# Kernel tuning notes

Measured on AMD Instinct MI355X. Metric: run time of the kernel, lower is better.

The kernel has to match this reference:

```python
import jax, jax.numpy as jnp
import numpy as np

IMG = 8       # image_size
LH = 150      # l_h
LQ = 10       # l_q
K = 10        # value-iteration steps
B = 16384     # batch
N_STATES = 2 + IMG * IMG


def _conv(x, w, pad):
    # NCHW conv, stride 1
    return jax.lax.conv_general_dilated(
        x, w, window_strides=(1, 1), padding=[(pad, pad), (pad, pad)],
        dimension_numbers=('NCHW', 'OIHW', 'NCHW'))


def setup_inputs() -> dict:
    key = jax.random.key(0)
    ks = jax.random.split(key, 8)
    grid = jax.random.normal(ks[0], (B, IMG * IMG), dtype=jnp.float32)
    pos = jax.random.randint(ks[1], (B, 2), 0, IMG).astype(jnp.float32)
    S = jnp.concatenate([grid, pos], axis=1)                      # [B, 66]
    Wh = jax.random.normal(ks[2], (LH, 1, 3, 3), jnp.float32) * 0.1
    bh = jnp.zeros((LH,), jnp.float32)
    Wr = jax.random.normal(ks[3], (1, LH, 1, 1), jnp.float32) * 0.1
    Wq = jax.random.normal(ks[4], (LQ, 1, 3, 3), jnp.float32) * 0.1
    w = jax.random.normal(ks[5], (LQ, 1, 3, 3), jnp.float32) * 0.1
    Wfc = jax.random.normal(ks[6], (8, LQ), jnp.float32) * 0.1
    return {'S': S, 'Wh': Wh, 'bh': bh, 'Wr': Wr, 'Wq': Wq, 'w': w, 'Wfc': Wfc}


def reference(S, Wh, bh, Wr, Wq, w, Wfc):
    X = S[:, :IMG * IMG].reshape(-1, 1, IMG, IMG)                 # [B,1,8,8]
    s1 = S[:, IMG * IMG].astype(jnp.int32)                        # row index
    s2 = S[:, IMG * IMG + 1].astype(jnp.int32)                    # col index

    h = _conv(X, Wh, 1) + bh[None, :, None, None]                 # [B,150,8,8]
    r = _conv(h, Wr, 0)                                           # [B,1,8,8]
    q = _conv(r, Wq, 1)                                           # [B,10,8,8]
    v = jnp.max(q, axis=1, keepdims=True)                         # [B,1,8,8]

    Wcat = jnp.concatenate([Wq, w], axis=1)                       # [10,2,3,3]

    def step(v, _):
        qq = _conv(jnp.concatenate([r, v], axis=1), Wcat, 1)
        return jnp.max(qq, axis=1, keepdims=True), None

    v, _ = jax.lax.scan(step, v, None, length=K - 1)
    q = _conv(jnp.concatenate([r, v], axis=1), Wcat, 1)           # [B,10,8,8]

    bidx = jnp.arange(q.shape[0])
    q_sel = q[bidx, :, s1, s2]                                    # [B,10]
    logits = q_sel @ Wfc.T                                        # [B,8]
    return logits
```

## Files before the change

kernel.cpp:

```cpp
#include <hip/hip_runtime.h>

#define IMG 8
#define LH 150
#define LQ 10
#define KITER 10
#define ROW (IMG * IMG + 2)

#define DPP_SHR1 0x111
#define DPP_SHL1 0x101
#define DPP_SHR8 0x118
#define DPP_SHL8 0x108
template <int CTRL>
__device__ __forceinline__ float dppf(float v) {
    return __builtin_bit_cast(float,
        __builtin_amdgcn_update_dpp(0, __builtin_bit_cast(int, v),
                                    CTRL, 0xF, 0xF, true));
}

__device__ __forceinline__ float bperm(int byte_addr, float v) {
    return __builtin_bit_cast(float,
        __builtin_amdgcn_ds_bpermute(byte_addr, __builtin_bit_cast(int, v)));
}

__global__ void weff_kernel(const float* __restrict__ Wh,
                            const float* __restrict__ bh,
                            const float* __restrict__ Wr,
                            float* __restrict__ ws) {
    const int wv = threadIdx.x >> 6;
    const int lane = threadIdx.x & 63;
    float partial = 0.f;
    for (int c = lane; c < LH; c += 64) {
        const float wr = Wr[c];
        partial += wr * ((wv < 9) ? Wh[c * 9 + wv] : bh[c]);
    }
    #pragma unroll
    for (int off = 32; off > 0; off >>= 1)
        partial += __shfl_xor(partial, off);
    if (lane == 0) ws[wv] = partial;
}

__global__ __launch_bounds__(256, 4) void vin_kernel(
    const float* __restrict__ S,
    const float* __restrict__ Wq,
    const float* __restrict__ w,
    const float* __restrict__ Wfc,
    const float* __restrict__ ws,
    float* __restrict__ out,
    int B) {
    const int wave = threadIdx.x >> 6;
    const int lane = threadIdx.x & 63;
    const long wid = (long)blockIdx.x * 4 + wave;
    if (wid * 4 >= B) return;

    const int x = lane & 7;
    const int ioff = (lane >> 4) * ROW;
    const float mskL = (x == 0) ? 0.f : 1.f;
    const float mskR = (x == 7) ? 0.f : 1.f;

    const float* Sb = S + wid * 4 * ROW;
    const int ybase = ((lane >> 3) & 1) * 32 + x;

    float X[4];
    #pragma unroll
    for (int yy = 0; yy < 4; ++yy) X[yy] = Sb[ioff + ybase + yy * 8];
    const int s1 = (int)Sb[ioff + 64];
    const int s2 = (int)Sb[ioff + 65];

    float C[6], L[6], R[6];
    auto expand = [&](const float V[4]) {
        C[0] = dppf<DPP_SHR8>(V[3]);
        C[1] = V[0]; C[2] = V[1]; C[3] = V[2]; C[4] = V[3];
        C[5] = dppf<DPP_SHL8>(V[0]);
        #pragma unroll
        for (int j = 0; j < 6; ++j) {
            L[j] = dppf<DPP_SHR1>(C[j]) * mskL;
            R[j] = dppf<DPP_SHL1>(C[j]) * mskR;
        }
    };
    auto conv9 = [&](int yy, const float* wt, float acc) {
        acc = fmaf(L[yy],     wt[0], acc);
        acc = fmaf(C[yy],     wt[1], acc);
        acc = fmaf(R[yy],     wt[2], acc);
        acc = fmaf(L[yy + 1], wt[3], acc);
        acc = fmaf(C[yy + 1], wt[4], acc);
        acc = fmaf(R[yy + 1], wt[5], acc);
        acc = fmaf(L[yy + 2], wt[6], acc);
        acc = fmaf(C[yy + 2], wt[7], acc);
        acc = fmaf(R[yy + 2], wt[8], acc);
        return acc;
    };

    expand(X);
    float r[4];
    #pragma unroll
    for (int yy = 0; yy < 4; ++yy) r[yy] = conv9(yy, ws, ws[9]);

    expand(r);
    float qr[LQ][4];
    #pragma unroll
    for (int o = 0; o < LQ; ++o)
        #pragma unroll
        for (int yy = 0; yy < 4; ++yy)
            qr[o][yy] = conv9(yy, Wq + o * 9, 0.f);

    float v[4];
    #pragma unroll
    for (int yy = 0; yy < 4; ++yy) {
        float m = qr[0][yy];
        #pragma unroll
        for (int o = 1; o < LQ; ++o) m = fmaxf(m, qr[o][yy]);
        v[yy] = m;
    }

    #pragma unroll 1
    for (int k = 0; k < KITER - 1; ++k) {
        expand(v);
        float m[4];
        #pragma unroll
        for (int o = 0; o < LQ; ++o) {
            #pragma unroll
            for (int yy = 0; yy < 4; ++yy) {
                const float acc = conv9(yy, w + o * 9, qr[o][yy]);
                m[yy] = (o == 0) ? acc : fmaxf(m[yy], acc);
            }
        }
        #pragma unroll
        for (int yy = 0; yy < 4; ++yy) v[yy] = m[yy];
    }

    float wfc[LQ];
    #pragma unroll
    for (int o = 0; o < LQ; ++o) wfc[o] = Wfc[x * LQ + o];

    expand(v);
    const bool sb0 = (s1 & 1) != 0, sb1 = (s1 & 2) != 0;
    const int selb = ((lane & 48) + (s1 >> 2) * 8 + s2) << 2;
    float logit = 0.f;
    #pragma unroll
    for (int o = 0; o < LQ; ++o) {
        float q[4];
        #pragma unroll
        for (int yy = 0; yy < 4; ++yy) q[yy] = conv9(yy, w + o * 9, qr[o][yy]);
        const float t0 = sb0 ? q[1] : q[0];
        const float t1 = sb0 ? q[3] : q[2];
        const float qy = sb1 ? t1 : t0;
        logit = fmaf(bperm(selb, qy), wfc[o], logit);
    }

    if ((lane & 8) == 0)
        out[wid * 32 + (lane >> 4) * 8 + x] = logit;
}

extern "C" void kernel_launch(void* const* d_in, const int* in_sizes, int n_in,
                              void* d_out, int out_size, void* d_ws, size_t ws_size,
                              hipStream_t stream) {
    const float* S   = (const float*)d_in[0];
    const float* Wh  = (const float*)d_in[1];
    const float* bh  = (const float*)d_in[2];
    const float* Wr  = (const float*)d_in[3];
    const float* Wq  = (const float*)d_in[4];
    const float* w   = (const float*)d_in[5];
    const float* Wfc = (const float*)d_in[6];
    float* out = (float*)d_out;
    float* ws  = (float*)d_ws;

    const int B = in_sizes[0] / ROW;

    weff_kernel<<<1, 640, 0, stream>>>(Wh, bh, Wr, ws);

    const int grid = (B + 15) / 16;
    vin_kernel<<<grid, 256, 0, stream>>>(S, Wq, w, Wfc, ws, out, B);
}
```

Baseline: 98.92 us.

## Fuse effective-weight reduction into main kernel and pair max tree in VI loop

Removes the separate single-block weff_kernel launch. Every wave now recomputes the 10 effective conv weights from Wh, bh and Wr using a per-lane partial sum and shuffle reduction. The max over the 10 channels is restructured into pairwise fmaxf, and the value-iteration loop is partially unrolled by 3, to expose more instruction-level parallelism. The cost is redundant per-wave reduction work (10 shuffle trees, 150*10 loads) and possibly higher register pressure from unrolling.

```diff
diff --git a/kernel.cpp b/kernel.cpp
--- a/kernel.cpp
+++ b/kernel.cpp
@@ -22,29 +22,14 @@
         __builtin_amdgcn_ds_bpermute(byte_addr, __builtin_bit_cast(int, v)));
 }
 
-__global__ void weff_kernel(const float* __restrict__ Wh,
-                            const float* __restrict__ bh,
-                            const float* __restrict__ Wr,
-                            float* __restrict__ ws) {
-    const int wv = threadIdx.x >> 6;
-    const int lane = threadIdx.x & 63;
-    float partial = 0.f;
-    for (int c = lane; c < LH; c += 64) {
-        const float wr = Wr[c];
-        partial += wr * ((wv < 9) ? Wh[c * 9 + wv] : bh[c]);
-    }
-    #pragma unroll
-    for (int off = 32; off > 0; off >>= 1)
-        partial += __shfl_xor(partial, off);
-    if (lane == 0) ws[wv] = partial;
-}
-
 __global__ __launch_bounds__(256, 4) void vin_kernel(
     const float* __restrict__ S,
+    const float* __restrict__ Wh,
+    const float* __restrict__ bh,
+    const float* __restrict__ Wr,
     const float* __restrict__ Wq,
     const float* __restrict__ w,
     const float* __restrict__ Wfc,
-    const float* __restrict__ ws,
     float* __restrict__ out,
     int B) {
     const int wave = threadIdx.x >> 6;
@@ -56,6 +41,21 @@
     const int ioff = (lane >> 4) * ROW;
     const float mskL = (x == 0) ? 0.f : 1.f;
     const float mskR = (x == 7) ? 0.f : 1.f;
+
+    float part[10];
+    #pragma unroll
+    for (int t = 0; t < 10; ++t) part[t] = 0.f;
+    for (int c = lane; c < LH; c += 64) {
+        const float wr = Wr[c];
+        #pragma unroll
+        for (int t = 0; t < 9; ++t) part[t] = fmaf(wr, Wh[c * 9 + t], part[t]);
+        part[9] = fmaf(wr, bh[c], part[9]);
+    }
+    #pragma unroll
+    for (int off = 32; off > 0; off >>= 1) {
+        #pragma unroll
+        for (int t = 0; t < 10; ++t) part[t] += __shfl_xor(part[t], off);
+    }
 
     const float* Sb = S + wid * 4 * ROW;
     const int ybase = ((lane >> 3) & 1) * 32 + x;
@@ -93,7 +93,7 @@
     expand(X);
     float r[4];
     #pragma unroll
-    for (int yy = 0; yy < 4; ++yy) r[yy] = conv9(yy, ws, ws[9]);
+    for (int yy = 0; yy < 4; ++yy) r[yy] = conv9(yy, part, part[9]);
 
     expand(r);
     float qr[LQ][4];
@@ -106,22 +106,30 @@
     float v[4];
     #pragma unroll
     for (int yy = 0; yy < 4; ++yy) {
-        float m = qr[0][yy];
+        float m = fmaxf(qr[0][yy], qr[1][yy]);
         #pragma unroll
-        for (int o = 1; o < LQ; ++o) m = fmaxf(m, qr[o][yy]);
+        for (int op = 1; op < 5; ++op)
+            m = fmaxf(m, fmaxf(qr[2 * op][yy], qr[2 * op + 1][yy]));
         v[yy] = m;
     }
 
-    #pragma unroll 1
+    #pragma unroll 3
     for (int k = 0; k < KITER - 1; ++k) {
         expand(v);
         float m[4];
         #pragma unroll
-        for (int o = 0; o < LQ; ++o) {
+        for (int op = 0; op < 5; ++op) {
+            float a0[4], a1[4];
+            #pragma unroll
+            for (int yy = 0; yy < 4; ++yy)
+                a0[yy] = conv9(yy, w + (2 * op) * 9, qr[2 * op][yy]);
+            #pragma unroll
+            for (int yy = 0; yy < 4; ++yy)
+                a1[yy] = conv9(yy, w + (2 * op + 1) * 9, qr[2 * op + 1][yy]);
             #pragma unroll
             for (int yy = 0; yy < 4; ++yy) {
-                const float acc = conv9(yy, w + o * 9, qr[o][yy]);
-                m[yy] = (o == 0) ? acc : fmaxf(m[yy], acc);
+                const float p = fmaxf(a0[yy], a1[yy]);
+                m[yy] = (op == 0) ? p : fmaxf(m[yy], p);
             }
         }
         #pragma unroll
@@ -162,12 +170,9 @@
     const float* w   = (const float*)d_in[5];
     const float* Wfc = (const float*)d_in[6];
     float* out = (float*)d_out;
-    float* ws  = (float*)d_ws;
 
     const int B = in_sizes[0] / ROW;
 
-    weff_kernel<<<1, 640, 0, stream>>>(Wh, bh, Wr, ws);
-
     const int grid = (B + 15) / 16;
-    vin_kernel<<<grid, 256, 0, stream>>>(S, Wq, w, Wfc, ws, out, B);
+    vin_kernel<<<grid, 256, 0, stream>>>(S, Wh, bh, Wr, Wq, w, Wfc, out, B);
 }
```

Result: no change. 98.88 us (-0.0%).
